# Optimization experiments

Measured on AMD Instinct MI355X. Metric: run time of the kernel, lower is better.

## Reference

```python
import jax, jax.numpy as jnp
import numpy as np
import math

B, S, D, H, V = 2, 2048, 512, 4, 32000
WINDOWS = [None, 128, 512, None]  # per-head attention windows (None = unlimited)


def setup_inputs() -> dict:
    key = jax.random.key(0)
    ks = jax.random.split(key, 8)
    input_ids = jax.random.randint(ks[0], (B, S), 0, V, dtype=jnp.int64)
    padding_mask = jnp.zeros((B, S), dtype=bool)  # True = pad
    embed_table = jax.random.normal(ks[1], (V, D), dtype=jnp.float32) * 0.02
    self_factors = jnp.full((H,), 0.1, dtype=jnp.float32)
    distance_alphas = jnp.full((H,), 0.1, dtype=jnp.float32)
    # torch Linear weights: [out_features, in_features], xavier-uniform init
    lim_f = math.sqrt(6.0 / (H * D + D))
    fusion_w = jax.random.uniform(ks[2], (D, H * D), jnp.float32, -lim_f, lim_f)
    fusion_b = jnp.zeros((D,), jnp.float32)
    lim_o = math.sqrt(6.0 / (D + V))
    out_w = jax.random.uniform(ks[3], (V, D), jnp.float32, -lim_o, lim_o)
    out_b = jnp.zeros((V,), jnp.float32)
    return {
        "input_ids": input_ids,
        "padding_mask": padding_mask,
        "embed_table": embed_table,
        "self_factors": self_factors,
        "distance_alphas": distance_alphas,
        "fusion_w": fusion_w,
        "fusion_b": fusion_b,
        "out_w": out_w,
        "out_b": out_b,
    }


def reference(input_ids, padding_mask, embed_table, self_factors,
              distance_alphas, fusion_w, fusion_b, out_w, out_b):
    b, s = input_ids.shape
    d = embed_table.shape[1]
    h = self_factors.shape[0]

    emb = embed_table[input_ids]  # [B,S,D]

    pos = jnp.arange(s)
    dist = jnp.abs(pos[:, None] - pos[None, :])          # [S,S]
    causal = pos[None, :] > pos[:, None]                  # [S,S] strict upper triangle
    eye = dist == 0                                       # [S,S]

    # shared raw scores, computed once (same for all heads)
    base = jnp.einsum('bqd,bkd->bqk', emb, emb) / math.sqrt(d)  # [B,S,S]

    # per-head distance decay bias: [H,S,S]
    decay = 1.0 / (1.0 + distance_alphas[:, None, None] * dist.astype(jnp.float32))

    scores = base[None, :, :, :] * decay[:, None, :, :]   # [H,B,S,S]
    # diagonal self-factor scaling
    scores = jnp.where(eye[None, None],
                       scores * self_factors[:, None, None, None], scores)

    # per-head window mask (None -> window >= S, never masks)
    win = jnp.array([s if w is None else w for w in WINDOWS[:h]])
    window_mask = dist[None, :, :] > win[:, None, None]   # [H,S,S]

    # key padding mask, diagonal exempted (as in original)
    key_pad = padding_mask[:, None, :] & (~eye[None])      # [B,S,S]

    full_mask = (window_mask[:, None] | causal[None, None] | key_pad[None])  # [H,B,S,S]
    scores = jnp.where(full_mask, -jnp.inf, scores)

    attn = jax.nn.softmax(scores, axis=-1)                 # [H,B,S,S]
    ctx = jnp.einsum('hbqk,bkd->hbqd', attn, emb)          # [H,B,S,D]

    concat = jnp.moveaxis(ctx, 0, 2).reshape(b, s, h * d)  # [B,S,H*D]
    fused = concat @ fusion_w.T + fusion_b                 # [B,S,D]
    logits = fused @ out_w.T + out_b                       # [B,S,V]
    return logits
```

## Files before the change

### kernel.cpp

```cpp
#include <hip/hip_runtime.h>
#include <hip/hip_bf16.h>
#include <stdint.h>

#define BB 2
#define SB 2048
#define DD 512
#define HH 4
#define VV 32000

typedef __attribute__((ext_vector_type(4))) float f32x4;
typedef __attribute__((ext_vector_type(8))) short bf16x8;
typedef __attribute__((ext_vector_type(4))) unsigned short us4;

__device__ __forceinline__ unsigned short f2bf(float f) {
    unsigned u = __float_as_uint(f);
    u += 0x7fffu + ((u >> 16) & 1u);
    return (unsigned short)(u >> 16);
}

__device__ __forceinline__ __attribute__((address_space(3))) unsigned int*
as_lds(void* p) {
    return (__attribute__((address_space(3))) unsigned int*)(unsigned)(uintptr_t)p;
}
__device__ __forceinline__ const __attribute__((address_space(1))) unsigned int*
as_gbl(const void* p) {
    return (const __attribute__((address_space(1))) unsigned int*)(uintptr_t)p;
}

__device__ __forceinline__ bf16x8 ldsrd64(const unsigned short* base, int row, int c) {
    return *(const bf16x8*)((const char*)base + row * 128 + ((c ^ (row & 7)) << 4));
}

__global__ void k_prep(const int* __restrict__ ids, const float* __restrict__ tbl,
                       const float* __restrict__ als,
                       const float* __restrict__ fw, const float* __restrict__ ow,
                       unsigned short* __restrict__ outw_bf, unsigned short* __restrict__ fusw_bf,
                       unsigned short* __restrict__ emb, unsigned short* __restrict__ embT,
                       float* __restrict__ dtab, float* __restrict__ lsum)
{
    __shared__ unsigned short TT[64][72];
    const int bid = blockIdx.x, t = threadIdx.x;

    if (bid < 2000) {
        int base = bid * 8192 + t * 4;
#pragma unroll
        for (int it = 0; it < 8; ++it) {
            int i = base + it * 1024;
            float4 v = *(const float4*)(ow + i);
            us4 o; o.x = f2bf(v.x); o.y = f2bf(v.y); o.z = f2bf(v.z); o.w = f2bf(v.w);
            *(us4*)(outw_bf + i) = o;
        }
    } else if (bid < 2256) {
        int base = (bid - 2000) * 4096 + t * 4;
#pragma unroll
        for (int it = 0; it < 4; ++it) {
            int i = base + it * 1024;
            float4 v = *(const float4*)(fw + i);
            us4 o; o.x = f2bf(v.x); o.y = f2bf(v.y); o.z = f2bf(v.z); o.w = f2bf(v.w);
            *(us4*)(fusw_bf + i) = o;
        }
    } else if (bid < 6352) {
        int row = bid - 2256;
        int id = ids[row];
        if (id < 0) id = 0;
        if (id >= VV) id = VV - 1;
        const float* s = tbl + (size_t)id * DD;
        unsigned short* d = emb + (size_t)row * DD;
        d[t]       = f2bf(s[t]);
        d[t + 256] = f2bf(s[t + 256]);
    } else if (bid < 6448) {
        int i = (bid - 6352) * 256 + t;
        if (i < HH * SB) {
            int h = i >> 11, dd = i & (SB - 1);
            dtab[i] = 0.04419417382415922f / (1.f + als[h] * (float)dd);
        } else {
            lsum[i - HH * SB] = 0.f;
        }
    } else {
        int bid2 = bid - 6448;
        const int d0 = (bid2 & 7) * 64, s0 = ((bid2 >> 3) & 31) * 64, b = bid2 >> 8;
        {
            int s = t >> 2, c16 = (t & 3) * 16;
            int id = ids[b * SB + s0 + s];
            if (id < 0) id = 0;
            if (id >= VV) id = VV - 1;
            const float* src = tbl + (size_t)id * DD + d0 + c16;
#pragma unroll
            for (int q4 = 0; q4 < 4; ++q4) {
                float4 v = *(const float4*)(src + q4 * 4);
                TT[c16 + q4 * 4 + 0][s] = f2bf(v.x);
                TT[c16 + q4 * 4 + 1][s] = f2bf(v.y);
                TT[c16 + q4 * 4 + 2][s] = f2bf(v.z);
                TT[c16 + q4 * 4 + 3][s] = f2bf(v.w);
            }
        }
        __syncthreads();
        {
            int d = t >> 2, sc = (t & 3) * 16;
            bf16x8 o0, o1;
#pragma unroll
            for (int j = 0; j < 8; ++j) {
                o0[j] = (short)TT[d][sc + j];
                o1[j] = (short)TT[d][sc + 8 + j];
            }
            unsigned short* dst = embT + ((size_t)(b * DD + d0 + d)) * SB + s0 + sc;
            *(bf16x8*)dst = o0;
            *(bf16x8*)(dst + 8) = o1;
        }
    }
}

__launch_bounds__(256, 2)
__global__ void k_base(const unsigned short* __restrict__ emb,
                       const unsigned char* __restrict__ pad,
                       const float* __restrict__ sfs,
                       const float* __restrict__ als,
                       const float* __restrict__ dtab,
                       unsigned short* __restrict__ P,
                       float* __restrict__ lsum)
{
    const int kt = blockIdx.x, qt = blockIdx.y, b = blockIdx.z;
    if (kt > qt + 1) return;
    const int tid = threadIdx.x, lane = tid & 63, wv = tid >> 6;
    const int l15 = lane & 15, g = lane >> 4;

    if (kt == qt + 1) {
        int row = tid >> 2, cb = (tid & 3) * 16;
        int4 z = {0, 0, 0, 0};
#pragma unroll
        for (int h = 0; h < 4; ++h) {
            unsigned short* Ph = P + (((size_t)(h * 2 + b)) * SB + qt * 64 + row) * SB + kt * 64 + cb;
            *(int4*)Ph = z;
            *(int4*)(Ph + 8) = z;
        }
        return;
    }

    __shared__ __align__(16) unsigned short Ql[2][64 * 128];
    __shared__ __align__(16) unsigned short Kl[2][64 * 128];

    const int q = qt * 64 + wv * 16 + l15;
    const bool dup = (sfs[0] == sfs[3]) && (als[0] == als[3]);

#define STAGEB(buf_, dc_) {                                                            \
    _Pragma("unroll")                                                                  \
    for (int i = 0; i < 4; ++i) {                                                      \
        int flat = (i * 256 + tid) * 8;                                                \
        int row = flat >> 7;                                                           \
        int ch  = (flat >> 3) & 15;                                                    \
        int scol = ((ch ^ (row & 15)) << 3);                                           \
        __builtin_amdgcn_global_load_lds(                                              \
            as_gbl(emb + ((size_t)(b * SB + qt * 64 + row)) * DD + (dc_) * 128 + scol),\
            as_lds(Ql[buf_] + flat), 16, 0, 0);                                        \
        __builtin_amdgcn_global_load_lds(                                              \
            as_gbl(emb + ((size_t)(b * SB + kt * 64 + row)) * DD + (dc_) * 128 + scol),\
            as_lds(Kl[buf_] + flat), 16, 0, 0);                                        \
    } }

    f32x4 zero4 = {0.f, 0.f, 0.f, 0.f};
    f32x4 cc[4];
#pragma unroll
    for (int c = 0; c < 4; ++c) cc[c] = zero4;

    STAGEB(0, 0);
    __syncthreads();
    for (int dc = 0; dc < 4; ++dc) {
        const int cur = dc & 1;
        if (dc < 3) STAGEB(cur ^ 1, dc + 1);
#pragma unroll
        for (int dsl = 0; dsl < 4; ++dsl) {
            int chr = (dsl * 4 + g);
            bf16x8 qf = *(const bf16x8*)(Ql[cur] + (wv * 16 + l15) * 128 + ((chr ^ l15) << 3));
#pragma unroll
            for (int c = 0; c < 4; ++c) {
                bf16x8 kf = *(const bf16x8*)(Kl[cur] + (c * 16 + l15) * 128 + ((chr ^ l15) << 3));
                cc[c] = __builtin_amdgcn_mfma_f32_16x16x32_bf16(kf, qf, cc[c], 0, 0, 0);
            }
        }
        __syncthreads();
    }
#undef STAGEB

    unsigned long long padm = __ballot(pad[(size_t)b * SB + kt * 64 + lane] != 0);

    const int wins[4] = {1 << 30, 128, 512, 1 << 30};
#pragma unroll
    for (int h = 0; h < 4; ++h) {
        if (h == 3 && dup) continue;
        const int win = wins[h];
        if (kt * 64 + win + 192 < qt * 64) continue;
        const float sf = sfs[h];
        const float* dth = dtab + h * SB;
        float rsum = 0.f;
        unsigned short pb[4][4];
#pragma unroll
        for (int c = 0; c < 4; ++c) {
#pragma unroll
            for (int r = 0; r < 4; ++r) {
                int kk = kt * 64 + c * 16 + 4 * g + r;
                int dist = q - kk;
                float p = 0.f;
                if (dist >= 0 && dist <= win &&
                    ((dist == 0) || !((padm >> (c * 16 + 4 * g + r)) & 1ull))) {
                    float s = cc[c][r] * dth[dist];
                    if (dist == 0) s *= sf;
                    p = __expf(s);
                }
                rsum += p;
                pb[c][r] = f2bf(p);
            }
        }
        unsigned short* Ph = P + (((size_t)(h * 2 + b)) * SB + q) * SB + kt * 64;
#pragma unroll
        for (int c = 0; c < 4; ++c) {
            us4 o;
            o.x = pb[c][0]; o.y = pb[c][1]; o.z = pb[c][2]; o.w = pb[c][3];
            *(us4*)(Ph + c * 16 + 4 * g) = o;
        }
        rsum += __shfl_xor(rsum, 16, 64);
        rsum += __shfl_xor(rsum, 32, 64);
        if (lane < 16)
            atomicAdd(&lsum[((size_t)(h * 2 + b)) * SB + q], rsum);
    }
}

__launch_bounds__(256, 2)
__global__ void k_pv(const unsigned short* __restrict__ P,
                     const unsigned short* __restrict__ embT,
                     const float* __restrict__ lsum,
                     const float* __restrict__ sfs,
                     const float* __restrict__ als,
                     unsigned short* __restrict__ concat)
{
    const int t64 = blockIdx.x, b = blockIdx.y, h = blockIdx.z;
    const bool dup = (sfs[0] == sfs[3]) && (als[0] == als[3]);
    if (h == 3 && dup) return;
    const int mt = t64 >> 2, nt = t64 & 3;
    const int Q0 = mt * 128;
    const int win = (h == 1) ? 128 : (h == 2) ? 512 : (1 << 30);
    int klo = Q0 - win - 64; if (klo < 0) klo = 0; klo &= ~63;
    const int khi = Q0 + 128;
    const int nsteps = (khi - klo) >> 6;

    __shared__ __align__(16) unsigned short Pl[2][128 * 64];
    __shared__ __align__(16) unsigned short Vl[2][128 * 64];

    const int tid = threadIdx.x, lane = tid & 63, wv = tid >> 6;
    const int wm = (wv >> 1) * 64, wn = (wv & 1) * 64;
    const int l15 = lane & 15, g = lane >> 4;

    f32x4 zero4 = {0.f, 0.f, 0.f, 0.f};
    f32x4 acc[4][4];
#pragma unroll
    for (int i = 0; i < 4; ++i)
#pragma unroll
        for (int j = 0; j < 4; ++j) acc[i][j] = zero4;

    const unsigned short* Ab = P + (((size_t)(h * 2 + b)) * SB + Q0) * SB;
    const unsigned short* Bb = embT + ((size_t)(b * DD + nt * 128)) * SB;

    const unsigned short* Ps[4];
    const unsigned short* Vs[4];
    int ldst[4];
#pragma unroll
    for (int j = 0; j < 4; ++j) {
        int ch = j * 256 + tid;
        int row = ch >> 3, cpos = ch & 7;
        int scol = ((cpos ^ (row & 7)) << 3);
        Ps[j] = Ab + (size_t)row * SB + scol;
        Vs[j] = Bb + (size_t)row * SB + scol;
        ldst[j] = ch * 16;
    }

#define STAGEPV(buf_, k0_) {                                                           \
    _Pragma("unroll")                                                                  \
    for (int j = 0; j < 4; ++j) {                                                      \
        __builtin_amdgcn_global_load_lds(as_gbl(Ps[j] + (k0_)),                        \
            as_lds((char*)Pl[buf_] + ldst[j]), 16, 0, 0);                              \
        __builtin_amdgcn_global_load_lds(as_gbl(Vs[j] + (k0_)),                        \
            as_lds((char*)Vl[buf_] + ldst[j]), 16, 0, 0);                              \
    } }

    STAGEPV(0, klo);
    __syncthreads();
    for (int t = 0; t < nsteps; ++t) {
        const int cur = t & 1;
        if (t + 1 < nsteps) STAGEPV(cur ^ 1, klo + (t + 1) * 64);
#pragma unroll
        for (int s = 0; s < 2; ++s) {
            bf16x8 af[4], bfr[4];
#pragma unroll
            for (int i = 0; i < 4; ++i) {
                af[i]  = ldsrd64(Pl[cur], wm + i * 16 + l15, s * 4 + g);
                bfr[i] = ldsrd64(Vl[cur], wn + i * 16 + l15, s * 4 + g);
            }
#pragma unroll
            for (int i = 0; i < 4; ++i)
#pragma unroll
                for (int j = 0; j < 4; ++j)
                    acc[i][j] = __builtin_amdgcn_mfma_f32_16x16x32_bf16(af[i], bfr[j], acc[i][j], 0, 0, 0);
        }
        __syncthreads();
    }
#undef STAGEPV

    const float* ls = lsum + ((size_t)(h * 2 + b)) * SB;
    unsigned short* cb  = concat + ((size_t)(b * SB)) * (HH * DD) + h * DD + nt * 128;
    unsigned short* cb3 = concat + ((size_t)(b * SB)) * (HH * DD) + 3 * DD + nt * 128;
    const bool wr3 = (h == 0) && dup;
#pragma unroll
    for (int i = 0; i < 4; ++i) {
        int rowb = wm + i * 16 + g * 4;
        float inv[4];
#pragma unroll
        for (int rr = 0; rr < 4; ++rr) inv[rr] = 1.f / ls[Q0 + rowb + rr];
#pragma unroll
        for (int j = 0; j < 4; ++j) {
            int col = wn + j * 16 + l15;
#pragma unroll
            for (int rr = 0; rr < 4; ++rr) {
                unsigned short v = f2bf(acc[i][j][rr] * inv[rr]);
                cb[(size_t)(Q0 + rowb + rr) * (HH * DD) + col] = v;
                if (wr3) cb3[(size_t)(Q0 + rowb + rr) * (HH * DD) + col] = v;
            }
        }
    }
}

template <int OUTF32>
__launch_bounds__(256, 2)
__global__ void k_gemm_bt(const unsigned short* __restrict__ A,
                          const unsigned short* __restrict__ Bt,
                          const float* __restrict__ bias,
                          void* __restrict__ Cout,
                          int M, int N, int K)
{
    const int nMt = M >> 7;
    const int nwg = gridDim.x;
    int bid = blockIdx.x;
    int q = nwg >> 3, r = nwg & 7;
    int x = bid & 7, o = bid >> 3;
    int wg = (x < r ? x * (q + 1) : r * (q + 1) + (x - r) * q) + o;
    const int mt = wg % nMt, nt = wg / nMt;

    __shared__ __align__(16) unsigned short Al[2][128 * 32];
    __shared__ __align__(16) unsigned short Bl[2][128 * 32];

    const int tid = threadIdx.x;
    const int lane = tid & 63;
    const int wv = tid >> 6;
    const int wm = (wv >> 1) * 64, wn = (wv & 1) * 64;
    const int l15 = lane & 15, g = lane >> 4;

    f32x4 zero4 = {0.f, 0.f, 0.f, 0.f};
    f32x4 acc[4][4];
#pragma unroll
    for (int i = 0; i < 4; ++i)
#pragma unroll
        for (int j = 0; j < 4; ++j) acc[i][j] = zero4;

    const unsigned short* Ab = A + (size_t)mt * 128 * K;
    const unsigned short* Bb = Bt + (size_t)nt * 128 * K;

#define STAGEF(buf_, k0_) {                                                            \
    _Pragma("unroll")                                                                  \
    for (int s = 0; s < 2; ++s) {                                                      \
        int e = (s * 256 + tid) * 8;                                                   \
        int row = e >> 5, col = e & 31;                                                \
        __builtin_amdgcn_global_load_lds(as_gbl(Ab + (size_t)row * K + (k0_) + col),   \
                                         as_lds(Al[buf_] + e), 16, 0, 0);              \
        __builtin_amdgcn_global_load_lds(as_gbl(Bb + (size_t)row * K + (k0_) + col),   \
                                         as_lds(Bl[buf_] + e), 16, 0, 0);              \
    } }

    const int nk = K >> 5;
    STAGEF(0, 0);
    __syncthreads();
    for (int t = 0; t < nk; ++t) {
        const int cur = t & 1;
        if (t + 1 < nk) STAGEF(cur ^ 1, (t + 1) * 32);
        bf16x8 af[4], bfr[4];
#pragma unroll
        for (int i = 0; i < 4; ++i) {
            af[i]  = *(const bf16x8*)(Al[cur] + (wm + i * 16 + l15) * 32 + 8 * g);
            bfr[i] = *(const bf16x8*)(Bl[cur] + (wn + i * 16 + l15) * 32 + 8 * g);
        }
#pragma unroll
        for (int i = 0; i < 4; ++i)
#pragma unroll
            for (int j = 0; j < 4; ++j)
                acc[i][j] = __builtin_amdgcn_mfma_f32_16x16x32_bf16(af[i], bfr[j], acc[i][j], 0, 0, 0);
        __syncthreads();
    }
#undef STAGEF

#pragma unroll
    for (int i = 0; i < 4; ++i) {
        int rowb = mt * 128 + wm + i * 16 + g * 4;
#pragma unroll
        for (int j = 0; j < 4; ++j) {
            int col = nt * 128 + wn + j * 16 + l15;
            float bv = bias[col];
            if (OUTF32) {
                float* C = (float*)Cout;
#pragma unroll
                for (int rr = 0; rr < 4; ++rr)
                    C[(size_t)(rowb + rr) * N + col] = acc[i][j][rr] + bv;
            } else {
                unsigned short* C = (unsigned short*)Cout;
#pragma unroll
                for (int rr = 0; rr < 4; ++rr)
                    C[(size_t)(rowb + rr) * N + col] = f2bf(acc[i][j][rr] + bv);
            }
        }
    }
}

__launch_bounds__(512, 1)
__global__ void k_logits(const unsigned short* __restrict__ A,
                         const unsigned short* __restrict__ Bt,
                         const float* __restrict__ bias,
                         float* __restrict__ Cout,
                         int M, int N, int K)
{
    const int nNt = (N + 255) >> 8;
    const int nwg = gridDim.x;
    int bid = blockIdx.x;
    int q = nwg >> 3, r = nwg & 7;
    int x = bid & 7, o = bid >> 3;
    int wg = (x < r ? x * (q + 1) : r * (q + 1) + (x - r) * q) + o;
    const int nt = wg % nNt, mt = wg / nNt;

    __shared__ __align__(16) char smem[131072];

    const int tid = threadIdx.x, lane = tid & 63, wv = tid >> 6;
    const int wr = wv >> 2, wc = wv & 3;
    const int l15 = lane & 15, g = lane >> 4;

    f32x4 zero4 = {0.f, 0.f, 0.f, 0.f};
    f32x4 acc[8][4];
#pragma unroll
    for (int i = 0; i < 8; ++i)
#pragma unroll
        for (int j = 0; j < 4; ++j) acc[i][j] = zero4;

    const unsigned short* Ab = A + (size_t)mt * 256 * K;
    const unsigned short* Bb = Bt + (size_t)nt * 256 * K;

    const unsigned short* As[4];
    const unsigned short* Bs[4];
    int ldstA[4], ldstB[4];
#pragma unroll
    for (int j = 0; j < 4; ++j) {
        int ch = tid + j * 512;
        int row = ch >> 3, cpos = ch & 7;
        int scol = ((cpos ^ (row & 7)) << 3);
        As[j] = Ab + (size_t)row * K + scol;
        Bs[j] = Bb + (size_t)row * K + scol;
        ldstA[j] = ch * 16;
        ldstB[j] = 65536 + ch * 16;
    }

#define STG(bufi_, k0_) {                                                              \
    _Pragma("unroll")                                                                  \
    for (int j = 0; j < 4; ++j)                                                        \
        __builtin_amdgcn_global_load_lds(as_gbl(As[j] + (k0_)),                        \
            as_lds(smem + (bufi_) * 32768 + ldstA[j]), 16, 0, 0);                      \
    _Pragma("unroll")                                                                  \
    for (int j = 0; j < 4; ++j)                                                        \
        __builtin_amdgcn_global_load_lds(as_gbl(Bs[j] + (k0_)),                        \
            as_lds(smem + (bufi_) * 32768 + ldstB[j]), 16, 0, 0); }

    STG(0, 0);
    __syncthreads();

    for (int t = 0; t < 8; ++t) {
        const int cur = t & 1;
        if (t < 7) STG(cur ^ 1, (t + 1) * 64);
        const unsigned short* Ar = (const unsigned short*)(smem + cur * 32768);
        const unsigned short* Br = (const unsigned short*)(smem + cur * 32768 + 65536);
#pragma unroll
        for (int s = 0; s < 2; ++s) {
            bf16x8 bf[4], af[8];
#pragma unroll
            for (int n = 0; n < 4; ++n)
                bf[n] = ldsrd64(Br, wc * 64 + n * 16 + l15, s * 4 + g);
#pragma unroll
            for (int m = 0; m < 8; ++m)
                af[m] = ldsrd64(Ar, wr * 128 + m * 16 + l15, s * 4 + g);
            __builtin_amdgcn_s_setprio(1);
#pragma unroll
            for (int m = 0; m < 8; ++m)
#pragma unroll
                for (int n = 0; n < 4; ++n)
                    acc[m][n] = __builtin_amdgcn_mfma_f32_16x16x32_bf16(af[m], bf[n], acc[m][n], 0, 0, 0);
            __builtin_amdgcn_s_setprio(0);
        }
        __syncthreads();
    }
#undef STG

    const int mrow = mt * 256;
    const int ncol = nt * 256;
    float* Cl = (float*)smem;
    float bvj[4];
#pragma unroll
    for (int j = 0; j < 4; ++j) bvj[j] = bias[ncol + wc * 64 + j * 16 + l15];
    const int srow = tid >> 4;
    const int scol = (tid & 15) * 4;
    const float* Crd = Cl + srow * 258 + scol;
#pragma unroll
    for (int mc = 0; mc < 8; ++mc) {
        if (wr == (mc >> 2)) {
            int ibase = (mc & 3) * 2;
#pragma unroll
            for (int ii = 0; ii < 2; ++ii) {
                int i = ibase + ii;
                int lr = ii * 16 + g * 4;
#pragma unroll
                for (int j = 0; j < 4; ++j)
#pragma unroll
                    for (int rr = 0; rr < 4; ++rr)
                        Cl[(lr + rr) * 258 + wc * 64 + j * 16 + l15] = acc[i][j][rr] + bvj[j];
            }
        }
        __syncthreads();
        {
            float* gp = Cout + (size_t)(mrow + mc * 32 + srow) * N + ncol + scol;
#pragma unroll
            for (int it = 0; it < 4; ++it)
                *(float4*)(gp + it * 64) = *(const float4*)(Crd + it * 64);
        }
        __syncthreads();
    }
}

extern "C" void kernel_launch(void* const* d_in, const int* in_sizes, int n_in,
                              void* d_out, int out_size, void* d_ws, size_t ws_size,
                              hipStream_t stream)
{
    const int*           ids = (const int*)d_in[0];
    const unsigned char* pad = (const unsigned char*)d_in[1];
    const float*         tbl = (const float*)d_in[2];
    const float*         sfs = (const float*)d_in[3];
    const float*         als = (const float*)d_in[4];
    const float*         fw  = (const float*)d_in[5];
    const float*         fb  = (const float*)d_in[6];
    const float*         ow  = (const float*)d_in[7];
    const float*         ob  = (const float*)d_in[8];
    float* logits = (float*)d_out;

    char* ws = (char*)d_ws;
    unsigned short* outw_bf = (unsigned short*)(ws);
    unsigned short* fusw_bf = (unsigned short*)(ws + 32768000);
    unsigned short* emb_bf  = (unsigned short*)(ws + 34865152);
    unsigned short* concat  = (unsigned short*)(ws + 39059456);
    unsigned short* fused   = (unsigned short*)(ws + 55836672);

    char* ob_scratch = (char*)d_out;
    unsigned short* P    = (unsigned short*)(ob_scratch);
    unsigned short* embT = (unsigned short*)(ob_scratch + 67108864);
    float*          dtab = (float*)(ob_scratch + 71303168);
    float*          lsum = (float*)(ob_scratch + 71335936);

    k_prep<<<6960, 256, 0, stream>>>(ids, tbl, als, fw, ow,
                                     outw_bf, fusw_bf, emb_bf, embT, dtab, lsum);

    dim3 bg(32, 32, BB);
    k_base<<<bg, 256, 0, stream>>>(emb_bf, pad, sfs, als, dtab, P, lsum);

    dim3 pg(64, BB, HH);
    k_pv<<<pg, 256, 0, stream>>>(P, embT, lsum, sfs, als, concat);

    k_gemm_bt<0><<<32 * 4, 256, 0, stream>>>(concat, fusw_bf, fb, fused, BB * SB, DD, HH * DD);
    k_logits<<<16 * 125, 512, 0, stream>>>(fused, outw_bf, ob, logits, BB * SB, VV, DD);
}
```

Before: 342.3 us.

## Shrink logits GEMM tile to 128x128 with 256-thread blocks and direct stores

Rewrites the output-projection GEMM to use 128x128 tiles, 4 waves per block, K-step 32 with double-buffered LDS, and two blocks per CU. The LDS-staged float4 epilogue is replaced by direct per-lane global stores with bias. The aim is higher occupancy and less epilogue sync overhead. The cost is more global reloads of operands, unswizzled LDS reads that may bank-conflict, and less coalesced output writes.

```diff
diff --git a/kernel.cpp b/kernel.cpp
--- a/kernel.cpp
+++ b/kernel.cpp
@@ -416,14 +416,14 @@
     }
 }
 
-__launch_bounds__(512, 1)
+__launch_bounds__(256, 2)
 __global__ void k_logits(const unsigned short* __restrict__ A,
                          const unsigned short* __restrict__ Bt,
                          const float* __restrict__ bias,
                          float* __restrict__ Cout,
                          int M, int N, int K)
 {
-    const int nNt = (N + 255) >> 8;
+    const int nNt = N >> 7;
     const int nwg = gridDim.x;
     int bid = blockIdx.x;
     int q = nwg >> 3, r = nwg & 7;
@@ -431,107 +431,70 @@
     int wg = (x < r ? x * (q + 1) : r * (q + 1) + (x - r) * q) + o;
     const int nt = wg % nNt, mt = wg / nNt;
 
-    __shared__ __align__(16) char smem[131072];
-
-    const int tid = threadIdx.x, lane = tid & 63, wv = tid >> 6;
-    const int wr = wv >> 2, wc = wv & 3;
+    __shared__ __align__(16) unsigned short Al[2][128 * 32];
+    __shared__ __align__(16) unsigned short Bl[2][128 * 32];
+
+    const int tid = threadIdx.x;
+    const int lane = tid & 63;
+    const int wv = tid >> 6;
+    const int wm = (wv >> 1) * 64, wn = (wv & 1) * 64;
     const int l15 = lane & 15, g = lane >> 4;
 
     f32x4 zero4 = {0.f, 0.f, 0.f, 0.f};
-    f32x4 acc[8][4];
-#pragma unroll
-    for (int i = 0; i < 8; ++i)
+    f32x4 acc[4][4];
+#pragma unroll
+    for (int i = 0; i < 4; ++i)
 #pragma unroll
         for (int j = 0; j < 4; ++j) acc[i][j] = zero4;
 
-    const unsigned short* Ab = A + (size_t)mt * 256 * K;
-    const unsigned short* Bb = Bt + (size_t)nt * 256 * K;
-
-    const unsigned short* As[4];
-    const unsigned short* Bs[4];
-    int ldstA[4], ldstB[4];
-#pragma unroll
-    for (int j = 0; j < 4; ++j) {
-        int ch = tid + j * 512;
-        int row = ch >> 3, cpos = ch & 7;
-        int scol = ((cpos ^ (row & 7)) << 3);
-        As[j] = Ab + (size_t)row * K + scol;
-        Bs[j] = Bb + (size_t)row * K + scol;
-        ldstA[j] = ch * 16;
-        ldstB[j] = 65536 + ch * 16;
-    }
-
-#define STG(bufi_, k0_) {                                                              \
+    const unsigned short* Ab = A + (size_t)mt * 128 * K;
+    const unsigned short* Bb = Bt + (size_t)nt * 128 * K;
+
+#define STG(buf_, k0_) {                                                               \
     _Pragma("unroll")                                                                  \
-    for (int j = 0; j < 4; ++j)                                                        \
-        __builtin_amdgcn_global_load_lds(as_gbl(As[j] + (k0_)),                        \
-            as_lds(smem + (bufi_) * 32768 + ldstA[j]), 16, 0, 0);                      \
-    _Pragma("unroll")                                                                  \
-    for (int j = 0; j < 4; ++j)                                                        \
-        __builtin_amdgcn_global_load_lds(as_gbl(Bs[j] + (k0_)),                        \
-            as_lds(smem + (bufi_) * 32768 + ldstB[j]), 16, 0, 0); }
-
+    for (int s = 0; s < 2; ++s) {                                                      \
+        int e = (s * 256 + tid) * 8;                                                   \
+        int row = e >> 5, col = e & 31;                                                \
+        __builtin_amdgcn_global_load_lds(as_gbl(Ab + (size_t)row * K + (k0_) + col),   \
+                                         as_lds(Al[buf_] + e), 16, 0, 0);              \
+        __builtin_amdgcn_global_load_lds(as_gbl(Bb + (size_t)row * K + (k0_) + col),   \
+                                         as_lds(Bl[buf_] + e), 16, 0, 0);              \
+    } }
+
+    const int nk = K >> 5;
     STG(0, 0);
     __syncthreads();
-
-    for (int t = 0; t < 8; ++t) {
+    for (int t = 0; t < nk; ++t) {
         const int cur = t & 1;
-        if (t < 7) STG(cur ^ 1, (t + 1) * 64);
-        const unsigned short* Ar = (const unsigned short*)(smem + cur * 32768);
-        const unsigned short* Br = (const unsigned short*)(smem + cur * 32768 + 65536);
-#pragma unroll
-        for (int s = 0; s < 2; ++s) {
-            bf16x8 bf[4], af[8];
-#pragma unroll
-            for (int n = 0; n < 4; ++n)
-                bf[n] = ldsrd64(Br, wc * 64 + n * 16 + l15, s * 4 + g);
-#pragma unroll
-            for (int m = 0; m < 8; ++m)
-                af[m] = ldsrd64(Ar, wr * 128 + m * 16 + l15, s * 4 + g);
-            __builtin_amdgcn_s_setprio(1);
-#pragma unroll
-            for (int m = 0; m < 8; ++m)
-#pragma unroll
-                for (int n = 0; n < 4; ++n)
-                    acc[m][n] = __builtin_amdgcn_mfma_f32_16x16x32_bf16(af[m], bf[n], acc[m][n], 0, 0, 0);
-            __builtin_amdgcn_s_setprio(0);
-        }
+        if (t + 1 < nk) STG(cur ^ 1, (t + 1) * 32);
+        bf16x8 af[4], bfr[4];
+#pragma unroll
+        for (int i = 0; i < 4; ++i) {
+            af[i]  = *(const bf16x8*)(Al[cur] + (wm + i * 16 + l15) * 32 + 8 * g);
+            bfr[i] = *(const bf16x8*)(Bl[cur] + (wn + i * 16 + l15) * 32 + 8 * g);
+        }
+        __builtin_amdgcn_s_setprio(1);
+#pragma unroll
+        for (int i = 0; i < 4; ++i)
+#pragma unroll
+            for (int j = 0; j < 4; ++j)
+                acc[i][j] = __builtin_amdgcn_mfma_f32_16x16x32_bf16(af[i], bfr[j], acc[i][j], 0, 0, 0);
+        __builtin_amdgcn_s_setprio(0);
         __syncthreads();
     }
 #undef STG
 
-    const int mrow = mt * 256;
-    const int ncol = nt * 256;
-    float* Cl = (float*)smem;
-    float bvj[4];
-#pragma unroll
-    for (int j = 0; j < 4; ++j) bvj[j] = bias[ncol + wc * 64 + j * 16 + l15];
-    const int srow = tid >> 4;
-    const int scol = (tid & 15) * 4;
-    const float* Crd = Cl + srow * 258 + scol;
-#pragma unroll
-    for (int mc = 0; mc < 8; ++mc) {
-        if (wr == (mc >> 2)) {
-            int ibase = (mc & 3) * 2;
-#pragma unroll
-            for (int ii = 0; ii < 2; ++ii) {
-                int i = ibase + ii;
-                int lr = ii * 16 + g * 4;
-#pragma unroll
-                for (int j = 0; j < 4; ++j)
-#pragma unroll
-                    for (int rr = 0; rr < 4; ++rr)
-                        Cl[(lr + rr) * 258 + wc * 64 + j * 16 + l15] = acc[i][j][rr] + bvj[j];
-            }
-        }
-        __syncthreads();
-        {
-            float* gp = Cout + (size_t)(mrow + mc * 32 + srow) * N + ncol + scol;
-#pragma unroll
-            for (int it = 0; it < 4; ++it)
-                *(float4*)(gp + it * 64) = *(const float4*)(Crd + it * 64);
-        }
-        __syncthreads();
+#pragma unroll
+    for (int i = 0; i < 4; ++i) {
+        int rowb = mt * 128 + wm + i * 16 + g * 4;
+#pragma unroll
+        for (int j = 0; j < 4; ++j) {
+            int col = nt * 128 + wn + j * 16 + l15;
+            float bv = bias[col];
+#pragma unroll
+            for (int rr = 0; rr < 4; ++rr)
+                Cout[(size_t)(rowb + rr) * N + col] = acc[i][j][rr] + bv;
+        }
     }
 }
 
@@ -573,5 +536,5 @@
     k_pv<<<pg, 256, 0, stream>>>(P, embT, lsum, sfs, als, concat);
 
     k_gemm_bt<0><<<32 * 4, 256, 0, stream>>>(concat, fusw_bf, fb, fused, BB * SB, DD, HH * DD);
-    k_logits<<<16 * 125, 512, 0, stream>>>(fused, outw_bf, ob, logits, BB * SB, VV, DD);
-}
+    k_logits<<<32 * 250, 256, 0, stream>>>(fused, outw_bf, ob, logits, BB * SB, VV, DD);
+}
```

Result: slower. 383.7 us (+12.1%).
